# Kernel optimization log

Hardware: AMD Instinct MI355X
Metric: run time of the kernel (lower is better)

The kernel has to match this reference:

```python
import jax, jax.numpy as jnp
import numpy as np

N, CIN, COUT, E, NDIR = 65536, 128, 128, 589824, 9


def sel_conv(x, src, dst, sel, W, b):
    # x: [N, Cin]; W: [D, Cin, Cout]; edges j->i: out[i] += x[j] @ W[sel]
    n = x.shape[0]
    xs = x[src]  # [E, Cin] gather
    out = jnp.zeros((n, W.shape[2]), x.dtype)
    for d in range(W.shape[0]):  # fixed small direction count (9 or 1)
        m = (sel == d).astype(x.dtype)[:, None]
        agg = jax.ops.segment_sum(xs * m, dst, num_segments=n)  # [N, Cin]
        out = out + agg @ W[d]
    return out + b


def bn_eval(x, g, be, rm, rv, eps=1e-5):
    return (x - rm) * (g * jax.lax.rsqrt(rv + eps)) + be


def setup_inputs() -> dict:
    key = jax.random.key(0)
    ks = jax.random.split(key, 24)
    s = 0.05
    inp = {
        "x": jax.random.normal(ks[0], (N, CIN), jnp.float32),
        "edge_index": jax.random.randint(ks[1], (2, E), 0, N),
        "selections": jax.random.randint(ks[2], (E,), 0, NDIR),
        "W1": jax.random.normal(ks[3], (NDIR, CIN, COUT), jnp.float32) * s,
        "b1": jax.random.normal(ks[4], (COUT,), jnp.float32) * s,
        "g1": 1.0 + jax.random.normal(ks[5], (COUT,), jnp.float32) * s,
        "be1": jax.random.normal(ks[6], (COUT,), jnp.float32) * s,
        "rm1": jax.random.normal(ks[7], (COUT,), jnp.float32) * s,
        "rv1": 0.5 + jax.random.uniform(ks[8], (COUT,), jnp.float32),
        "W2": jax.random.normal(ks[9], (NDIR, COUT, COUT), jnp.float32) * s,
        "b2": jax.random.normal(ks[10], (COUT,), jnp.float32) * s,
        "g2": 1.0 + jax.random.normal(ks[11], (COUT,), jnp.float32) * s,
        "be2": jax.random.normal(ks[12], (COUT,), jnp.float32) * s,
        "rm2": jax.random.normal(ks[13], (COUT,), jnp.float32) * s,
        "rv2": 0.5 + jax.random.uniform(ks[14], (COUT,), jnp.float32),
        "W3": jax.random.normal(ks[15], (1, CIN, COUT), jnp.float32) * s,
        "b3": jax.random.normal(ks[16], (COUT,), jnp.float32) * s,
        "g3": 1.0 + jax.random.normal(ks[17], (COUT,), jnp.float32) * s,
        "be3": jax.random.normal(ks[18], (COUT,), jnp.float32) * s,
        "rm3": jax.random.normal(ks[19], (COUT,), jnp.float32) * s,
        "rv3": 0.5 + jax.random.uniform(ks[20], (COUT,), jnp.float32),
    }
    return inp


def reference(x, edge_index, selections, W1, b1, g1, be1, rm1, rv1,
              W2, b2, g2, be2, rm2, rv2, W3, b3, g3, be3, rm3, rv3):
    src, dst = edge_index[0], edge_index[1]
    # conv1: SelectionConv(3x3) + BN + ELU
    h = jax.nn.elu(bn_eval(sel_conv(x, src, dst, selections, W1, b1), g1, be1, rm1, rv1))
    # conv2: SelectionConv(3x3) + BN + ELU
    h = jax.nn.elu(bn_eval(sel_conv(h, src, dst, selections, W2, b2), g2, be2, rm2, rv2))
    # conv3: SelectionConv(1x1) shortcut (only selection-0 edges)
    sc = sel_conv(x, src, dst, selections, W3, b3)
    return jax.nn.elu(bn_eval(h + sc, g3, be3, rm3, rv3))
```

## Files before the change

### kernel.cpp

```cpp
#include <hip/hip_runtime.h>
#include <hip/hip_bf16.h>
#include <math.h>

#define N_NODES 65536
#define NDIR 9
#define NEDGE 589824
#define NBINS (N_NODES*NDIR)
#define TILE_M 32
#define SKEY_CAP 1024

typedef __attribute__((ext_vector_type(8))) short short8;
typedef __attribute__((ext_vector_type(4))) float f32x4;

__device__ inline float bf2f(unsigned short u){ return __uint_as_float(((unsigned int)u)<<16); }
__device__ inline unsigned short f2bf(float f){
  unsigned int x = __float_as_uint(f);
  x += 0x7fff + ((x>>16)&1);
  return (unsigned short)(x>>16);
}
__device__ inline float elu1(float x){ return x>0.f ? x : expm1f(x); }

__global__ void prep_w(const float* __restrict__ W1, const float* __restrict__ W2,
                       const float* __restrict__ W3,
                       const float* __restrict__ g1, const float* __restrict__ rv1,
                       const float* __restrict__ g2, const float* __restrict__ rv2,
                       const float* __restrict__ g3, const float* __restrict__ rv3,
                       unsigned short* __restrict__ Wt1, unsigned short* __restrict__ Wt2){
  int idx = blockIdx.x*256 + threadIdx.x;
  const float eps = 1e-5f;
  if (idx < 1280*128) {
    int n = idx >> 7, k = idx & 127;
    float v;
    if (n < 1152) { int d = n >> 7, c = n & 127;
      float s = g1[c]*rsqrtf(rv1[c]+eps); v = W1[(d*128 + k)*128 + c] * s; }
    else { int c = n - 1152;
      float s = g3[c]*rsqrtf(rv3[c]+eps); v = W3[k*128 + c] * s; }
    Wt1[idx] = f2bf(v);
  } else {
    int j = idx - 1280*128;
    int n = j >> 7, k = j & 127;
    int d = n >> 7, c = n & 127;
    float s = g2[c]*rsqrtf(rv2[c]+eps);
    Wt2[j] = f2bf(W2[(d*128 + k)*128 + c] * s);
  }
}

__global__ void prep_bias(const float* b1,const float* g1,const float* be1,const float* rm1,const float* rv1,
                          const float* b2,const float* g2,const float* be2,const float* rm2,const float* rv2,
                          const float* b3,const float* g3,const float* be3,const float* rm3,const float* rv3,
                          float* bias1, float* bias2, float* bias3, float* s3v){
  int c = threadIdx.x;
  const float eps = 1e-5f;
  float s1 = g1[c]*rsqrtf(rv1[c]+eps);
  bias1[c] = (b1[c]-rm1[c])*s1 + be1[c];
  float s2 = g2[c]*rsqrtf(rv2[c]+eps);
  bias2[c] = (b2[c]-rm2[c])*s2 + be2[c];
  float s3 = g3[c]*rsqrtf(rv3[c]+eps);
  bias3[c] = (b3[c]-rm3[c])*s3 + be3[c];
  s3v[c] = s3;
}

__global__ void xcast_k(const float* __restrict__ x, unsigned short* __restrict__ xb){
  int i = (blockIdx.x*256 + threadIdx.x)*8;
  f32x4 f0 = *(const f32x4*)(x + i);
  f32x4 f1 = *(const f32x4*)(x + i + 4);
  short8 t;
  #pragma unroll
  for (int j = 0; j < 4; j++){ t[j] = (short)f2bf(f0[j]); t[4+j] = (short)f2bf(f1[j]); }
  *(short8*)(xb + i) = t;
}

__global__ void hist_k(const int* __restrict__ dst, const int* __restrict__ sel,
                       int* __restrict__ hist){
  int e = blockIdx.x*256 + threadIdx.x;
  atomicAdd(&hist[dst[e]*9 + sel[e]], 1);
}

__global__ void scan1_k(const int* __restrict__ in, int* __restrict__ out, int* __restrict__ bsum){
  __shared__ int wsum[4];
  int t = threadIdx.x;
  int base = blockIdx.x*1024 + t*4;
  int4 v = *(const int4*)(in + base);
  int s = v.x + v.y + v.z + v.w;
  int lane = t & 63, w = t >> 6;
  int inc = s;
  #pragma unroll
  for (int o = 1; o < 64; o <<= 1){ int n = __shfl_up(inc, o); if (lane >= o) inc += n; }
  if (lane == 63) wsum[w] = inc;
  __syncthreads();
  int acc = 0;
  for (int i = 0; i < w; i++) acc += wsum[i];
  int ex = acc + inc - s;
  out[base] = ex; out[base+1] = ex + v.x; out[base+2] = ex + v.x + v.y; out[base+3] = ex + v.x + v.y + v.z;
  if (t == 255) bsum[blockIdx.x] = acc + inc;
}

__global__ void scan3_k(int* __restrict__ rs, const int* __restrict__ bsumx, int* __restrict__ cursor){
  int i = blockIdx.x*256 + threadIdx.x;
  int v = rs[i] + bsumx[i >> 10];
  rs[i] = v; cursor[i] = v;
  if (i == 0) rs[NBINS] = NEDGE;
}

__global__ void scatter_k(const int* __restrict__ src, const int* __restrict__ dst,
                          const int* __restrict__ sel,
                          int* __restrict__ cursor, int* __restrict__ sorted){
  int e = blockIdx.x*256 + threadIdx.x;
  int bin = dst[e]*9 + sel[e];
  int pos = atomicAdd(&cursor[bin], 1);
  sorted[pos] = src[e];
}

__device__ __forceinline__ void mfma_tile(f32x4 acc[2][2],
                                          const unsigned short* agg,
                                          const unsigned short* __restrict__ Wd,
                                          int w, int q, int r){
  #pragma unroll
  for (int kk = 0; kk < 4; kk++){
    const unsigned short* wp = Wd + (size_t)(w*32 + r)*128 + kk*32 + q*8;
    short8 b0 = *(const short8*)wp;
    short8 b1 = *(const short8*)(wp + 16*128);
    #pragma unroll
    for (int mt = 0; mt < 2; mt++){
      short8 av = *(const short8*)&agg[(mt*16 + r)*136 + kk*32 + q*8];
      acc[mt][0] = __builtin_amdgcn_mfma_f32_16x16x32_bf16(av, b0, acc[mt][0], 0, 0, 0);
      acc[mt][1] = __builtin_amdgcn_mfma_f32_16x16x32_bf16(av, b1, acc[mt][1], 0, 0, 0);
    }
  }
}

template<int IS_L2>
__global__ __launch_bounds__(256, 8) void layer_k(
    const unsigned short* __restrict__ H,
    const unsigned short* __restrict__ X,
    const unsigned short* __restrict__ Wf,
    const unsigned short* __restrict__ W3f,
    const int* __restrict__ rs, const int* __restrict__ sorted,
    const float* __restrict__ biasA, const float* __restrict__ bias3,
    const float* __restrict__ s3v,
    unsigned short* __restrict__ outB, float* __restrict__ outF){
  __shared__ __align__(16) unsigned short agg[TILE_M*136];
  __shared__ int skey[SKEY_CAP];
  __shared__ int rsl[TILE_M*9 + 1];
  const int tid = threadIdx.x;
  const int w = tid >> 6, lane = tid & 63;
  const int q = lane >> 4, r = lane & 15;
  const int rid = tid >> 4, c = tid & 15;
  const int m0 = blockIdx.x * TILE_M;

  for (int i = tid; i <= TILE_M*9; i += 256) rsl[i] = rs[m0*9 + i];
  __syncthreads();
  const int lo = rsl[0];
  const int cnt = rsl[TILE_M*9] - lo;
  for (int i = tid; i < cnt && i < SKEY_CAP; i += 256) skey[i] = sorted[lo + i];

  f32x4 acc[2][2];
  #pragma unroll
  for (int mt = 0; mt < 2; mt++){ acc[mt][0] = (f32x4){0,0,0,0}; acc[mt][1] = (f32x4){0,0,0,0}; }

  #pragma unroll 1
  for (int d = 0; d < 9; d++){
    __syncthreads();
    #pragma unroll
    for (int t = 0; t < 2; t++){
      int nl = t*16 + rid;
      int b = nl*9 + d;
      int s = rsl[b] - lo, e = rsl[b+1] - lo;
      f32x4 a0 = {0,0,0,0}, a1 = {0,0,0,0};
      for (int i = s; i < e; i++){
        int key = (i < SKEY_CAP) ? skey[i] : sorted[lo + i];
        short8 v = *(const short8*)(H + (size_t)key*128 + c*8);
        a0[0] += bf2f((unsigned short)v[0]); a0[1] += bf2f((unsigned short)v[1]);
        a0[2] += bf2f((unsigned short)v[2]); a0[3] += bf2f((unsigned short)v[3]);
        a1[0] += bf2f((unsigned short)v[4]); a1[1] += bf2f((unsigned short)v[5]);
        a1[2] += bf2f((unsigned short)v[6]); a1[3] += bf2f((unsigned short)v[7]);
      }
      short8 o;
      o[0]=(short)f2bf(a0[0]); o[1]=(short)f2bf(a0[1]); o[2]=(short)f2bf(a0[2]); o[3]=(short)f2bf(a0[3]);
      o[4]=(short)f2bf(a1[0]); o[5]=(short)f2bf(a1[1]); o[6]=(short)f2bf(a1[2]); o[7]=(short)f2bf(a1[3]);
      *(short8*)&agg[nl*136 + c*8] = o;
    }
    __syncthreads();
    mfma_tile(acc, agg, Wf + (size_t)d*128*128, w, q, r);
  }

  if constexpr (!IS_L2){
    #pragma unroll
    for (int mt = 0; mt < 2; mt++)
      #pragma unroll
      for (int n2 = 0; n2 < 2; n2++){
        int col = w*32 + n2*16 + r;
        float bA = biasA[col];
        #pragma unroll
        for (int rr = 0; rr < 4; rr++){
          int row = m0 + mt*16 + q*4 + rr;
          outB[(size_t)row*128 + col] = f2bf(elu1(acc[mt][n2][rr] + bA));
        }
      }
  } else {
    f32x4 sca[2][2];
    #pragma unroll
    for (int mt = 0; mt < 2; mt++){ sca[mt][0] = (f32x4){0,0,0,0}; sca[mt][1] = (f32x4){0,0,0,0}; }
    __syncthreads();
    #pragma unroll
    for (int t = 0; t < 2; t++){
      int nl = t*16 + rid;
      int b = nl*9;
      int s = rsl[b] - lo, e = rsl[b+1] - lo;
      f32x4 a0 = {0,0,0,0}, a1 = {0,0,0,0};
      for (int i = s; i < e; i++){
        int key = (i < SKEY_CAP) ? skey[i] : sorted[lo + i];
        short8 v = *(const short8*)(X + (size_t)key*128 + c*8);
        a0[0] += bf2f((unsigned short)v[0]); a0[1] += bf2f((unsigned short)v[1]);
        a0[2] += bf2f((unsigned short)v[2]); a0[3] += bf2f((unsigned short)v[3]);
        a1[0] += bf2f((unsigned short)v[4]); a1[1] += bf2f((unsigned short)v[5]);
        a1[2] += bf2f((unsigned short)v[6]); a1[3] += bf2f((unsigned short)v[7]);
      }
      short8 o;
      o[0]=(short)f2bf(a0[0]); o[1]=(short)f2bf(a0[1]); o[2]=(short)f2bf(a0[2]); o[3]=(short)f2bf(a0[3]);
      o[4]=(short)f2bf(a1[0]); o[5]=(short)f2bf(a1[1]); o[6]=(short)f2bf(a1[2]); o[7]=(short)f2bf(a1[3]);
      *(short8*)&agg[nl*136 + c*8] = o;
    }
    __syncthreads();
    mfma_tile(sca, agg, W3f, w, q, r);
    #pragma unroll
    for (int mt = 0; mt < 2; mt++)
      #pragma unroll
      for (int n2 = 0; n2 < 2; n2++){
        int col = w*32 + n2*16 + r;
        float bA = biasA[col], b3 = bias3[col], s3 = s3v[col];
        #pragma unroll
        for (int rr = 0; rr < 4; rr++){
          int row = m0 + mt*16 + q*4 + rr;
          float h = elu1(acc[mt][n2][rr] + bA);
          outF[(size_t)row*128 + col] = elu1(h*s3 + sca[mt][n2][rr] + b3);
        }
      }
  }
}

extern "C" void kernel_launch(void* const* d_in, const int* in_sizes, int n_in,
                              void* d_out, int out_size, void* d_ws, size_t ws_size,
                              hipStream_t stream){
  const float* x   = (const float*)d_in[0];
  const int*   ei  = (const int*)d_in[1];
  const int*   sel = (const int*)d_in[2];
  const float* W1  = (const float*)d_in[3];
  const float* b1  = (const float*)d_in[4];
  const float* g1  = (const float*)d_in[5];
  const float* be1 = (const float*)d_in[6];
  const float* rm1 = (const float*)d_in[7];
  const float* rv1 = (const float*)d_in[8];
  const float* W2  = (const float*)d_in[9];
  const float* b2  = (const float*)d_in[10];
  const float* g2  = (const float*)d_in[11];
  const float* be2 = (const float*)d_in[12];
  const float* rm2 = (const float*)d_in[13];
  const float* rv2 = (const float*)d_in[14];
  const float* W3  = (const float*)d_in[15];
  const float* b3  = (const float*)d_in[16];
  const float* g3  = (const float*)d_in[17];
  const float* be3 = (const float*)d_in[18];
  const float* rm3 = (const float*)d_in[19];
  const float* rv3 = (const float*)d_in[20];

  char* ws = (char*)d_ws;
  unsigned short* xb   = (unsigned short*)(ws);
  unsigned short* h1   = (unsigned short*)(ws + 16777216);
  unsigned short* Wt1  = (unsigned short*)(ws + 33554432);
  unsigned short* Wt2  = (unsigned short*)(ws + 33882112);
  float* bias1  = (float*)(ws + 34177024);
  float* bias2  = bias1 + 128;
  float* bias3  = bias1 + 256;
  float* s3v    = bias1 + 384;
  int* hist     = (int*)(ws + 34179072);
  int* rs       = (int*)(ws + 36538368);
  int* cursor   = (int*)(ws + 38897920);
  int* bsum     = (int*)(ws + 41257216);
  int* bsumx    = (int*)(ws + 41261312);
  int* bsumT    = (int*)(ws + 41265408);
  int* sorted   = (int*)(ws + 41265664);

  const int* srcp = ei;
  const int* dstp = ei + NEDGE;

  hipMemsetAsync(hist, 0, NBINS*sizeof(int), stream);
  prep_w<<<1216, 256, 0, stream>>>(W1, W2, W3, g1, rv1, g2, rv2, g3, rv3, Wt1, Wt2);
  prep_bias<<<1, 128, 0, stream>>>(b1,g1,be1,rm1,rv1, b2,g2,be2,rm2,rv2, b3,g3,be3,rm3,rv3,
                                   bias1, bias2, bias3, s3v);
  xcast_k<<<4096, 256, 0, stream>>>(x, xb);
  hist_k<<<NEDGE/256, 256, 0, stream>>>(dstp, sel, hist);
  scan1_k<<<NBINS/1024, 256, 0, stream>>>(hist, rs, bsum);
  scan1_k<<<1, 256, 0, stream>>>(bsum, bsumx, bsumT);
  scan3_k<<<NBINS/256, 256, 0, stream>>>(rs, bsumx, cursor);
  scatter_k<<<NEDGE/256, 256, 0, stream>>>(srcp, dstp, sel, cursor, sorted);

  layer_k<0><<<2048, 256, 0, stream>>>(xb, nullptr, Wt1, nullptr, rs, sorted,
                                       bias1, nullptr, nullptr, h1, nullptr);
  layer_k<1><<<2048, 256, 0, stream>>>(h1, xb, Wt2, Wt1 + 1152*128, rs, sorted,
                                       bias2, bias3, s3v, nullptr, (float*)d_out);
}
```

Measured before the change: 372.7 us.

## Fuse prep kernels, interleave per-row gathers, fold shortcut into accumulator

Four preprocessing launches (memset, weight prep, bias prep, x cast) are merged into one kernel to cut launch overhead. The gather loop now has each thread own 4 rows at 4 channels each and interleave their edge loads, which gives more memory-level parallelism per thread. The layer-2 shortcut becomes a tenth phase that applies ELU, scale and bias to the accumulator and then MFMAs the shortcut into it, removing a second set of accumulators. SKEY_CAP is halved to cut shared memory, at the cost of more fallback global reads for dense tiles.

```diff
diff --git a/kernel.cpp b/kernel.cpp
--- a/kernel.cpp
+++ b/kernel.cpp
@@ -7,7 +7,7 @@
 #define NEDGE 589824
 #define NBINS (N_NODES*NDIR)
 #define TILE_M 32
-#define SKEY_CAP 1024
+#define SKEY_CAP 512
 
 typedef __attribute__((ext_vector_type(8))) short short8;
 typedef __attribute__((ext_vector_type(4))) float f32x4;
@@ -20,15 +20,22 @@
 }
 __device__ inline float elu1(float x){ return x>0.f ? x : expm1f(x); }
 
-__global__ void prep_w(const float* __restrict__ W1, const float* __restrict__ W2,
-                       const float* __restrict__ W3,
-                       const float* __restrict__ g1, const float* __restrict__ rv1,
-                       const float* __restrict__ g2, const float* __restrict__ rv2,
-                       const float* __restrict__ g3, const float* __restrict__ rv3,
-                       unsigned short* __restrict__ Wt1, unsigned short* __restrict__ Wt2){
+__global__ void prep_all(const float* __restrict__ x,
+                         const float* __restrict__ W1, const float* __restrict__ W2,
+                         const float* __restrict__ W3,
+                         const float* __restrict__ b1, const float* __restrict__ g1,
+                         const float* __restrict__ be1, const float* __restrict__ rm1, const float* __restrict__ rv1,
+                         const float* __restrict__ b2, const float* __restrict__ g2,
+                         const float* __restrict__ be2, const float* __restrict__ rm2, const float* __restrict__ rv2,
+                         const float* __restrict__ b3, const float* __restrict__ g3,
+                         const float* __restrict__ be3, const float* __restrict__ rm3, const float* __restrict__ rv3,
+                         unsigned short* __restrict__ Wt1, unsigned short* __restrict__ Wt2,
+                         float* __restrict__ bias1, float* __restrict__ bias2,
+                         float* __restrict__ bias3, float* __restrict__ s3v,
+                         int* __restrict__ hist, unsigned short* __restrict__ xb){
   int idx = blockIdx.x*256 + threadIdx.x;
   const float eps = 1e-5f;
-  if (idx < 1280*128) {
+  if (idx < 163840) {
     int n = idx >> 7, k = idx & 127;
     float v;
     if (n < 1152) { int d = n >> 7, c = n & 127;
@@ -36,38 +43,35 @@
     else { int c = n - 1152;
       float s = g3[c]*rsqrtf(rv3[c]+eps); v = W3[k*128 + c] * s; }
     Wt1[idx] = f2bf(v);
-  } else {
-    int j = idx - 1280*128;
+  } else if (idx < 311296) {
+    int j = idx - 163840;
     int n = j >> 7, k = j & 127;
     int d = n >> 7, c = n & 127;
     float s = g2[c]*rsqrtf(rv2[c]+eps);
     Wt2[j] = f2bf(W2[(d*128 + k)*128 + c] * s);
+  } else if (idx < 311424) {
+    int c = idx - 311296;
+    float s1 = g1[c]*rsqrtf(rv1[c]+eps);
+    bias1[c] = (b1[c]-rm1[c])*s1 + be1[c];
+    float s2 = g2[c]*rsqrtf(rv2[c]+eps);
+    bias2[c] = (b2[c]-rm2[c])*s2 + be2[c];
+    float s3 = g3[c]*rsqrtf(rv3[c]+eps);
+    bias3[c] = (b3[c]-rm3[c])*s3 + be3[c];
+    s3v[c] = s3;
+  } else if (idx < 311424 + NBINS) {
+    hist[idx - 311424] = 0;
+  } else {
+    int j = idx - (311424 + NBINS);
+    if (j < N_NODES*16) {
+      int i = j*8;
+      f32x4 f0 = *(const f32x4*)(x + i);
+      f32x4 f1 = *(const f32x4*)(x + i + 4);
+      short8 t;
+      #pragma unroll
+      for (int jj = 0; jj < 4; jj++){ t[jj] = (short)f2bf(f0[jj]); t[4+jj] = (short)f2bf(f1[jj]); }
+      *(short8*)(xb + i) = t;
+    }
   }
-}
-
-__global__ void prep_bias(const float* b1,const float* g1,const float* be1,const float* rm1,const float* rv1,
-                          const float* b2,const float* g2,const float* be2,const float* rm2,const float* rv2,
-                          const float* b3,const float* g3,const float* be3,const float* rm3,const float* rv3,
-                          float* bias1, float* bias2, float* bias3, float* s3v){
-  int c = threadIdx.x;
-  const float eps = 1e-5f;
-  float s1 = g1[c]*rsqrtf(rv1[c]+eps);
-  bias1[c] = (b1[c]-rm1[c])*s1 + be1[c];
-  float s2 = g2[c]*rsqrtf(rv2[c]+eps);
-  bias2[c] = (b2[c]-rm2[c])*s2 + be2[c];
-  float s3 = g3[c]*rsqrtf(rv3[c]+eps);
-  bias3[c] = (b3[c]-rm3[c])*s3 + be3[c];
-  s3v[c] = s3;
-}
-
-__global__ void xcast_k(const float* __restrict__ x, unsigned short* __restrict__ xb){
-  int i = (blockIdx.x*256 + threadIdx.x)*8;
-  f32x4 f0 = *(const f32x4*)(x + i);
-  f32x4 f1 = *(const f32x4*)(x + i + 4);
-  short8 t;
-  #pragma unroll
-  for (int j = 0; j < 4; j++){ t[j] = (short)f2bf(f0[j]); t[4+j] = (short)f2bf(f1[j]); }
-  *(short8*)(xb + i) = t;
 }
 
 __global__ void hist_k(const int* __restrict__ dst, const int* __restrict__ sel,
@@ -145,7 +149,7 @@
   const int tid = threadIdx.x;
   const int w = tid >> 6, lane = tid & 63;
   const int q = lane >> 4, r = lane & 15;
-  const int rid = tid >> 4, c = tid & 15;
+  const int g8 = tid >> 5, c8 = tid & 31;
   const int m0 = blockIdx.x * TILE_M;
 
   for (int i = tid; i <= TILE_M*9; i += 256) rsl[i] = rs[m0*9 + i];
@@ -158,30 +162,62 @@
   #pragma unroll
   for (int mt = 0; mt < 2; mt++){ acc[mt][0] = (f32x4){0,0,0,0}; acc[mt][1] = (f32x4){0,0,0,0}; }
 
+  const int NPH = IS_L2 ? 10 : 9;
   #pragma unroll 1
-  for (int d = 0; d < 9; d++){
+  for (int d = 0; d < NPH; d++){
+    const bool scph = IS_L2 && (d == 9);
+    const unsigned short* T = scph ? X : H;
+    const int dd = scph ? 0 : d;
     __syncthreads();
-    #pragma unroll
-    for (int t = 0; t < 2; t++){
-      int nl = t*16 + rid;
-      int b = nl*9 + d;
-      int s = rsl[b] - lo, e = rsl[b+1] - lo;
-      f32x4 a0 = {0,0,0,0}, a1 = {0,0,0,0};
-      for (int i = s; i < e; i++){
-        int key = (i < SKEY_CAP) ? skey[i] : sorted[lo + i];
-        short8 v = *(const short8*)(H + (size_t)key*128 + c*8);
-        a0[0] += bf2f((unsigned short)v[0]); a0[1] += bf2f((unsigned short)v[1]);
-        a0[2] += bf2f((unsigned short)v[2]); a0[3] += bf2f((unsigned short)v[3]);
-        a1[0] += bf2f((unsigned short)v[4]); a1[1] += bf2f((unsigned short)v[5]);
-        a1[2] += bf2f((unsigned short)v[6]); a1[3] += bf2f((unsigned short)v[7]);
+
+    int s[4], e[4];
+    #pragma unroll
+    for (int t = 0; t < 4; t++){
+      int b = (g8 + 8*t)*9 + dd;
+      s[t] = rsl[b] - lo; e[t] = rsl[b+1] - lo;
+    }
+    f32x4 A[4];
+    #pragma unroll
+    for (int t = 0; t < 4; t++) A[t] = (f32x4){0,0,0,0};
+    int n = max(max(e[0]-s[0], e[1]-s[1]), max(e[2]-s[2], e[3]-s[3]));
+    for (int k = 0; k < n; k++){
+      #pragma unroll
+      for (int t = 0; t < 4; t++){
+        int i = s[t] + k;
+        if (i < e[t]){
+          int key = (i < SKEY_CAP) ? skey[i] : sorted[lo + i];
+          uint2 v = *(const uint2*)(T + (size_t)key*128 + c8*4);
+          A[t][0] += bf2f((unsigned short)(v.x & 0xffff));
+          A[t][1] += bf2f((unsigned short)(v.x >> 16));
+          A[t][2] += bf2f((unsigned short)(v.y & 0xffff));
+          A[t][3] += bf2f((unsigned short)(v.y >> 16));
+        }
       }
-      short8 o;
-      o[0]=(short)f2bf(a0[0]); o[1]=(short)f2bf(a0[1]); o[2]=(short)f2bf(a0[2]); o[3]=(short)f2bf(a0[3]);
-      o[4]=(short)f2bf(a1[0]); o[5]=(short)f2bf(a1[1]); o[6]=(short)f2bf(a1[2]); o[7]=(short)f2bf(a1[3]);
-      *(short8*)&agg[nl*136 + c*8] = o;
+    }
+    #pragma unroll
+    for (int t = 0; t < 4; t++){
+      unsigned int p0 = (unsigned int)f2bf(A[t][0]) | ((unsigned int)f2bf(A[t][1]) << 16);
+      unsigned int p1 = (unsigned int)f2bf(A[t][2]) | ((unsigned int)f2bf(A[t][3]) << 16);
+      uint2 o = {p0, p1};
+      *(uint2*)(agg + (size_t)(g8 + 8*t)*136 + c8*4) = o;
     }
     __syncthreads();
-    mfma_tile(acc, agg, Wf + (size_t)d*128*128, w, q, r);
+
+    if (scph){
+      #pragma unroll
+      for (int mt = 0; mt < 2; mt++)
+        #pragma unroll
+        for (int n2 = 0; n2 < 2; n2++){
+          int col = w*32 + n2*16 + r;
+          float bA = biasA[col], b3 = bias3[col], s3 = s3v[col];
+          #pragma unroll
+          for (int rr = 0; rr < 4; rr++)
+            acc[mt][n2][rr] = elu1(acc[mt][n2][rr] + bA)*s3 + b3;
+        }
+      mfma_tile(acc, agg, W3f, w, q, r);
+    } else {
+      mfma_tile(acc, agg, Wf + (size_t)dd*128*128, w, q, r);
+    }
   }
 
   if constexpr (!IS_L2){
@@ -198,42 +234,15 @@
         }
       }
   } else {
-    f32x4 sca[2][2];
-    #pragma unroll
-    for (int mt = 0; mt < 2; mt++){ sca[mt][0] = (f32x4){0,0,0,0}; sca[mt][1] = (f32x4){0,0,0,0}; }
-    __syncthreads();
-    #pragma unroll
-    for (int t = 0; t < 2; t++){
-      int nl = t*16 + rid;
-      int b = nl*9;
-      int s = rsl[b] - lo, e = rsl[b+1] - lo;
-      f32x4 a0 = {0,0,0,0}, a1 = {0,0,0,0};
-      for (int i = s; i < e; i++){
-        int key = (i < SKEY_CAP) ? skey[i] : sorted[lo + i];
-        short8 v = *(const short8*)(X + (size_t)key*128 + c*8);
-        a0[0] += bf2f((unsigned short)v[0]); a0[1] += bf2f((unsigned short)v[1]);
-        a0[2] += bf2f((unsigned short)v[2]); a0[3] += bf2f((unsigned short)v[3]);
-        a1[0] += bf2f((unsigned short)v[4]); a1[1] += bf2f((unsigned short)v[5]);
-        a1[2] += bf2f((unsigned short)v[6]); a1[3] += bf2f((unsigned short)v[7]);
-      }
-      short8 o;
-      o[0]=(short)f2bf(a0[0]); o[1]=(short)f2bf(a0[1]); o[2]=(short)f2bf(a0[2]); o[3]=(short)f2bf(a0[3]);
-      o[4]=(short)f2bf(a1[0]); o[5]=(short)f2bf(a1[1]); o[6]=(short)f2bf(a1[2]); o[7]=(short)f2bf(a1[3]);
-      *(short8*)&agg[nl*136 + c*8] = o;
-    }
-    __syncthreads();
-    mfma_tile(sca, agg, W3f, w, q, r);
     #pragma unroll
     for (int mt = 0; mt < 2; mt++)
       #pragma unroll
       for (int n2 = 0; n2 < 2; n2++){
         int col = w*32 + n2*16 + r;
-        float bA = biasA[col], b3 = bias3[col], s3 = s3v[col];
         #pragma unroll
         for (int rr = 0; rr < 4; rr++){
           int row = m0 + mt*16 + q*4 + rr;
-          float h = elu1(acc[mt][n2][rr] + bA);
-          outF[(size_t)row*128 + col] = elu1(h*s3 + sca[mt][n2][rr] + b3);
+          outF[(size_t)row*128 + col] = elu1(acc[mt][n2][rr]);
         }
       }
   }
@@ -284,11 +293,9 @@
   const int* srcp = ei;
   const int* dstp = ei + NEDGE;
 
-  hipMemsetAsync(hist, 0, NBINS*sizeof(int), stream);
-  prep_w<<<1216, 256, 0, stream>>>(W1, W2, W3, g1, rv1, g2, rv2, g3, rv3, Wt1, Wt2);
-  prep_bias<<<1, 128, 0, stream>>>(b1,g1,be1,rm1,rv1, b2,g2,be2,rm2,rv2, b3,g3,be3,rm3,rv3,
-                                   bias1, bias2, bias3, s3v);
-  xcast_k<<<4096, 256, 0, stream>>>(x, xb);
+  prep_all<<<(163840+147456+128+NBINS+N_NODES*16+255)/256, 256, 0, stream>>>(
+      x, W1, W2, W3, b1,g1,be1,rm1,rv1, b2,g2,be2,rm2,rv2, b3,g3,be3,rm3,rv3,
+      Wt1, Wt2, bias1, bias2, bias3, s3v, hist, xb);
   hist_k<<<NEDGE/256, 256, 0, stream>>>(dstp, sel, hist);
   scan1_k<<<NBINS/1024, 256, 0, stream>>>(hist, rs, bsum);
   scan1_k<<<1, 256, 0, stream>>>(bsum, bsumx, bsumT);
```

Measured after the change: 638.3 us. 1.71x slower.
